# Kernel optimization log

Hardware: AMD Instinct MI355X
Metric: run time of the kernel (lower is better)

The kernel has to match this reference:

```python
import jax, jax.numpy as jnp
import numpy as np

EMBED = 1024
HEADS = 16
HEAD_DIM = EMBED // HEADS
HIDDEN = 4 * EMBED
EPS = 1e-6


def setup_inputs() -> dict:
    key = jax.random.key(0)
    ks = jax.random.split(key, 8)
    s = 0.02
    return {
        "x": jax.random.normal(ks[0], (2, 2048, EMBED), dtype=jnp.float32),
        "ln1_w": jnp.ones((EMBED,), jnp.float32),
        "ln1_b": jnp.zeros((EMBED,), jnp.float32),
        "qkv_w": jax.random.normal(ks[1], (3 * EMBED, EMBED), jnp.float32) * s,
        "qkv_b": jnp.zeros((3 * EMBED,), jnp.float32),
        "proj_w": jax.random.normal(ks[2], (EMBED, EMBED), jnp.float32) * s,
        "proj_b": jnp.zeros((EMBED,), jnp.float32),
        "ln2_w": jnp.ones((EMBED,), jnp.float32),
        "ln2_b": jnp.zeros((EMBED,), jnp.float32),
        "fc1_w": jax.random.normal(ks[3], (HIDDEN, EMBED), jnp.float32) * s,
        "fc1_b": jnp.zeros((HIDDEN,), jnp.float32),
        "fc2_w": jax.random.normal(ks[4], (EMBED, HIDDEN), jnp.float32) * s,
        "fc2_b": jnp.zeros((EMBED,), jnp.float32),
    }


def _layernorm(x, w, b):
    mu = jnp.mean(x, axis=-1, keepdims=True)
    var = jnp.mean(jnp.square(x - mu), axis=-1, keepdims=True)
    return (x - mu) * jax.lax.rsqrt(var + EPS) * w + b


def _attn(x, qkv_w, qkv_b, proj_w, proj_b):
    B, S, E = x.shape
    qkv = x @ qkv_w.T + qkv_b                      # [B,S,3E]
    qkv = qkv.reshape(B, S, 3, HEADS, HEAD_DIM)
    q, k, v = jnp.moveaxis(qkv, 2, 0)              # each [B,S,H,D]
    q = q.transpose(0, 2, 1, 3)                    # [B,H,S,D]
    k = k.transpose(0, 2, 1, 3)
    v = v.transpose(0, 2, 1, 3)
    scale = HEAD_DIM ** -0.5
    scores = jnp.einsum("bhqd,bhkd->bhqk", q, k) * scale
    mask = jnp.tril(jnp.ones((S, S), dtype=bool))
    scores = jnp.where(mask, scores, -jnp.inf)
    attn = jax.nn.softmax(scores, axis=-1)
    out = jnp.einsum("bhqk,bhkd->bhqd", attn, v)   # [B,H,S,D]
    out = out.transpose(0, 2, 1, 3).reshape(B, S, E)
    return out @ proj_w.T + proj_b


def reference(x, ln1_w, ln1_b, qkv_w, qkv_b, proj_w, proj_b,
              ln2_w, ln2_b, fc1_w, fc1_b, fc2_w, fc2_b):
    x = x + _attn(_layernorm(x, ln1_w, ln1_b), qkv_w, qkv_b, proj_w, proj_b)
    h = _layernorm(x, ln2_w, ln2_b)
    h = jax.nn.gelu(h @ fc1_w.T + fc1_b, approximate=False)
    x = x + (h @ fc2_w.T + fc2_b)
    return x
```

## Files before the change

### kernel.cpp

```cpp
#include <hip/hip_runtime.h>
#include <hip/hip_bf16.h>


#define E_    1024
#define TE_   3072
#define S_    2048
#define B_    2
#define H_    16
#define MROWS 4096

typedef __attribute__((ext_vector_type(8))) short bf16x8;
typedef __attribute__((ext_vector_type(4))) short short4v;
typedef __attribute__((ext_vector_type(4))) float f32x4;

__device__ __forceinline__ short f2bf(float f) {
  union { float f; unsigned u; } v; v.f = f;
  unsigned r = v.u + 0x7fffu + ((v.u >> 16) & 1u);
  return (short)(r >> 16);
}
__device__ __forceinline__ float bf2f(short s) {
  union { unsigned u; float f; } v; v.u = ((unsigned)(unsigned short)s) << 16;
  return v.f;
}
__device__ __forceinline__ void gload_lds16(const void* g, void* l) {
  __builtin_amdgcn_global_load_lds(
      (const __attribute__((address_space(1))) unsigned int*)g,
      (__attribute__((address_space(3))) unsigned int*)l, 16, 0, 0);
}
__device__ __forceinline__ float exp2_fast(float x) {
  float r; asm("v_exp_f32 %0, %1" : "=v"(r) : "v"(x)); return r;
}
__device__ __forceinline__ float gelu_f(float v) {
  return 0.5f * v * (1.0f + erff(v * 0.70710678118654752f));
}

__global__ __launch_bounds__(256) void k_cvt4(const float* __restrict__ i0, short* __restrict__ o0, int n0,
                                              const float* __restrict__ i1, short* __restrict__ o1, int n1,
                                              const float* __restrict__ i2, short* __restrict__ o2, int n2,
                                              const float* __restrict__ i3, short* __restrict__ o3, int n3) {
  const float* in; short* out; int n;
  switch (blockIdx.y) {
    case 0: in = i0; out = o0; n = n0; break;
    case 1: in = i1; out = o1; n = n1; break;
    case 2: in = i2; out = o2; n = n2; break;
    default: in = i3; out = o3; n = n3; break;
  }
  int i = blockIdx.x * 256 + threadIdx.x;
  if (i >= n) return;
  float4 v = ((const float4*)in)[i];
  short4v o = { f2bf(v.x), f2bf(v.y), f2bf(v.z), f2bf(v.w) };
  ((short4v*)out)[i] = o;
}

__global__ __launch_bounds__(256) void k_ln(const float* __restrict__ x,
                                            const float* __restrict__ w,
                                            const float* __restrict__ b,
                                            short* __restrict__ out) {
  int row = blockIdx.x;
  int tid = threadIdx.x;
  float4 v = ((const float4*)(x + (size_t)row * E_))[tid];
  float s  = v.x + v.y + v.z + v.w;
  float s2 = v.x*v.x + v.y*v.y + v.z*v.z + v.w*v.w;
  #pragma unroll
  for (int d = 1; d < 64; d <<= 1) { s += __shfl_xor(s, d); s2 += __shfl_xor(s2, d); }
  __shared__ float rs[4], rq[4];
  int wv = tid >> 6;
  if ((tid & 63) == 0) { rs[wv] = s; rq[wv] = s2; }
  __syncthreads();
  s  = rs[0] + rs[1] + rs[2] + rs[3];
  s2 = rq[0] + rq[1] + rq[2] + rq[3];
  float mu  = s * (1.0f / E_);
  float var = fmaxf(s2 * (1.0f / E_) - mu * mu, 0.0f);
  float inv = rsqrtf(var + 1e-6f);
  float4 wv4 = ((const float4*)w)[tid];
  float4 bv4 = ((const float4*)b)[tid];
  short4v o = { f2bf((v.x - mu) * inv * wv4.x + bv4.x),
                f2bf((v.y - mu) * inv * wv4.y + bv4.y),
                f2bf((v.z - mu) * inv * wv4.z + bv4.z),
                f2bf((v.w - mu) * inv * wv4.w + bv4.w) };
  ((short4v*)(out + (size_t)row * E_))[tid] = o;
}

template <int EPI>
__global__ __launch_bounds__(256) void k_gemm(const short* __restrict__ A,
                                              const short* __restrict__ W,
                                              const float* __restrict__ bias,
                                              const float* __restrict__ res,
                                              void* __restrict__ outv,
                                              int M, int N, int K) {
  __shared__ short As[128 * 32];
  __shared__ short Ws[128 * 32];
  int tid  = threadIdx.x;
  int lane = tid & 63, wave = tid >> 6;
  int wm = wave >> 1, wn = wave & 1;
  int m0 = blockIdx.y * 128, n0 = blockIdx.x * 128;
  int fr = lane & 15, fq = lane >> 4, fk = fq * 8;

  f32x4 acc[4][4];
  #pragma unroll
  for (int i = 0; i < 4; ++i)
    #pragma unroll
    for (int j = 0; j < 4; ++j) acc[i][j] = (f32x4){0.f, 0.f, 0.f, 0.f};

  int sr = tid >> 2;
  int sc = (tid & 3) * 8;
  const short* Arow  = A + (size_t)(m0 + sr) * K + sc;
  const short* Wrow  = W + (size_t)(n0 + sr) * K + sc;
  const short* Arow2 = A + (size_t)(m0 + 64 + sr) * K + sc;
  const short* Wrow2 = W + (size_t)(n0 + 64 + sr) * K + sc;
  short* Asl = As + tid * 8;
  short* Wsl = Ws + tid * 8;

  for (int k0 = 0; k0 < K; k0 += 32) {
    __syncthreads();
    gload_lds16(Arow  + k0, Asl);
    gload_lds16(Wrow  + k0, Wsl);
    gload_lds16(Arow2 + k0, Asl + 2048);
    gload_lds16(Wrow2 + k0, Wsl + 2048);
    __syncthreads();
    bf16x8 af[4], bfr[4];
    #pragma unroll
    for (int i = 0; i < 4; ++i) {
      af[i]  = *(const bf16x8*)(As + (wm * 64 + i * 16 + fr) * 32 + fk);
      bfr[i] = *(const bf16x8*)(Ws + (wn * 64 + i * 16 + fr) * 32 + fk);
    }
    #pragma unroll
    for (int mi = 0; mi < 4; ++mi)
      #pragma unroll
      for (int ni = 0; ni < 4; ++ni)
        acc[mi][ni] = __builtin_amdgcn_mfma_f32_16x16x32_bf16(af[mi], bfr[ni],
                                                              acc[mi][ni], 0, 0, 0);
  }

  #pragma unroll
  for (int mi = 0; mi < 4; ++mi) {
    #pragma unroll
    for (int ni = 0; ni < 4; ++ni) {
      int gm0 = m0 + wm * 64 + mi * 16 + fq * 4;
      int gn  = n0 + wn * 64 + ni * 16 + fr;
      float bv = bias[gn];
      #pragma unroll
      for (int j = 0; j < 4; ++j) {
        size_t idx = (size_t)(gm0 + j) * N + gn;
        float v = acc[mi][ni][j] + bv;
        if (EPI == 0)      ((short*)outv)[idx] = f2bf(v);
        else if (EPI == 1) ((float*)outv)[idx] = v + res[idx];
        else               ((short*)outv)[idx] = f2bf(gelu_f(v));
      }
    }
  }
}

__global__ __launch_bounds__(256) void k_attn(const short* __restrict__ qkv,
                                              short* __restrict__ out) {
  __shared__ short Kt[64 * 64];
  __shared__ short Vt[64 * 64];
  __shared__ short Pl[4][1024];
  int tid  = threadIdx.x;
  int lane = tid & 63, w = tid >> 6;
  int qb   = (int)gridDim.x - 1 - (int)blockIdx.x;
  int q0   = qb * 64;
  int bh   = blockIdx.y;
  int b    = bh >> 4, h = bh & 15;
  int fr   = lane & 15, fq = lane >> 4, fk = fq * 8;
  const float sc = 0.18033688011112042f;

  const short* qp = qkv + (size_t)(b * S_ + q0 + w * 16 + fr) * TE_ + h * 64;
  bf16x8 qa0 = *(const bf16x8*)(qp + fk);
  bf16x8 qa1 = *(const bf16x8*)(qp + 32 + fk);

  float m_r = -__builtin_inff();
  float l_r = 0.f;
  f32x4 o[4];
  #pragma unroll
  for (int c = 0; c < 4; ++c) o[c] = (f32x4){0.f, 0.f, 0.f, 0.f};

  int srow = tid >> 3;
  int schunk = tid & 7;
  short* Pw = &Pl[w][0];

  for (int kv = 0; kv <= q0; kv += 64) {
    __syncthreads();
    #pragma unroll
    for (int r = 0; r < 2; ++r) {
      int row = srow + 32 * r;
      size_t grow = (size_t)(b * S_ + kv + row) * TE_ + h * 64;
      gload_lds16(qkv + grow + E_ + ((schunk ^ (srow & 7)) << 3),
                  Kt + r * 2048 + tid * 8);
      bf16x8 vv = *(const bf16x8*)(qkv + grow + 2 * E_ + (schunk << 3));
      int kc = row >> 3, kwi = row & 7;
      #pragma unroll
      for (int j = 0; j < 8; ++j) {
        int d = (schunk << 3) + j;
        int csw = kc ^ (d & 7) ^ ((d >> 3) & 7);
        Vt[d * 64 + csw * 8 + kwi] = vv[j];
      }
    }
    __syncthreads();

    f32x4 s[4];
    #pragma unroll
    for (int g = 0; g < 4; ++g) {
      const short* kb = Kt + ((g << 4) + fr) * 64;
      int sw = fr & 7;
      bf16x8 a0 = *(const bf16x8*)(kb + ((fq ^ sw) << 3));
      bf16x8 a1 = *(const bf16x8*)(kb + (((4 + fq) ^ sw) << 3));
      f32x4 t = (f32x4){0.f, 0.f, 0.f, 0.f};
      t = __builtin_amdgcn_mfma_f32_16x16x32_bf16(a0, qa0, t, 0, 0, 0);
      t = __builtin_amdgcn_mfma_f32_16x16x32_bf16(a1, qa1, t, 0, 0, 0);
      s[g] = t;
    }
    #pragma unroll
    for (int g = 0; g < 4; ++g)
      #pragma unroll
      for (int jj = 0; jj < 4; ++jj) s[g][jj] *= sc;

    if (kv + 64 > q0) {
      int qr = (q0 - kv) + 16 * w + fr;
      #pragma unroll
      for (int g = 0; g < 4; ++g)
        #pragma unroll
        for (int jj = 0; jj < 4; ++jj)
          if (16 * g + 4 * fq + jj > qr) s[g][jj] = -__builtin_inff();
    }

    float mg0 = fmaxf(fmaxf(s[0][0], s[0][1]), fmaxf(s[0][2], s[0][3]));
    float mg1 = fmaxf(fmaxf(s[1][0], s[1][1]), fmaxf(s[1][2], s[1][3]));
    float mg2 = fmaxf(fmaxf(s[2][0], s[2][1]), fmaxf(s[2][2], s[2][3]));
    float mg3 = fmaxf(fmaxf(s[3][0], s[3][1]), fmaxf(s[3][2], s[3][3]));
    float mt = fmaxf(fmaxf(mg0, mg1), fmaxf(mg2, mg3));
    mt = fmaxf(mt, __shfl_xor(mt, 16));
    mt = fmaxf(mt, __shfl_xor(mt, 32));
    float mn = fmaxf(m_r, mt);
    float al = exp2_fast(m_r - mn);
    m_r = mn;
    #pragma unroll
    for (int g = 0; g < 4; ++g)
      #pragma unroll
      for (int jj = 0; jj < 4; ++jj) s[g][jj] = exp2_fast(s[g][jj] - mn);
    f32x4 s4 = s[0] + s[1] + s[2] + s[3];
    float ps = (s4[0] + s4[1]) + (s4[2] + s4[3]);
    ps += __shfl_xor(ps, 16);
    ps += __shfl_xor(ps, 32);
    l_r = l_r * al + ps;

    #pragma unroll
    for (int g = 0; g < 4; ++g) {
      short4v pk = { f2bf(s[g][0]), f2bf(s[g][1]), f2bf(s[g][2]), f2bf(s[g][3]) };
      int pc = (2 * g + (fq >> 1)) ^ (fr & 7);
      *(short4v*)(Pw + fr * 64 + pc * 8 + ((fq & 1) << 2)) = pk;
    }

    #pragma unroll
    for (int c = 0; c < 4; ++c)
      #pragma unroll
      for (int jj = 0; jj < 4; ++jj) o[c][jj] *= al;

    bf16x8 pb0 = *(const bf16x8*)(Pw + fr * 64 + ((fq ^ (fr & 7)) << 3));
    bf16x8 pb1 = *(const bf16x8*)(Pw + fr * 64 + (((4 + fq) ^ (fr & 7)) << 3));
    #pragma unroll
    for (int c = 0; c < 4; ++c) {
      int d = 16 * c + fr;
      int sbase = (d & 7) ^ ((d >> 3) & 7);
      const short* vb = Vt + d * 64;
      bf16x8 va0 = *(const bf16x8*)(vb + ((fq ^ sbase) << 3));
      bf16x8 va1 = *(const bf16x8*)(vb + (((4 + fq) ^ sbase) << 3));
      o[c] = __builtin_amdgcn_mfma_f32_16x16x32_bf16(va0, pb0, o[c], 0, 0, 0);
      o[c] = __builtin_amdgcn_mfma_f32_16x16x32_bf16(va1, pb1, o[c], 0, 0, 0);
    }
  }

  float inv_l = 1.0f / l_r;
  #pragma unroll
  for (int c = 0; c < 4; ++c) {
    short4v okk = { f2bf(o[c][0] * inv_l), f2bf(o[c][1] * inv_l),
                    f2bf(o[c][2] * inv_l), f2bf(o[c][3] * inv_l) };
    int pc = (2 * c + (fq >> 1)) ^ (fr & 7);
    *(short4v*)(Pw + fr * 64 + pc * 8 + ((fq & 1) << 2)) = okk;
  }
  int ql = lane >> 2, dc = lane & 3;
  int swz = ql & 7;
  const short* ob = Pw + ql * 64;
  bf16x8 r0 = *(const bf16x8*)(ob + (((2 * dc) ^ swz) << 3));
  bf16x8 r1 = *(const bf16x8*)(ob + (((2 * dc + 1) ^ swz) << 3));
  short* op = out + (size_t)(b * S_ + q0 + 16 * w + ql) * E_ + h * 64 + dc * 16;
  *(bf16x8*)op = r0;
  *(bf16x8*)(op + 8) = r1;
}

extern "C" void kernel_launch(void* const* d_in, const int* in_sizes, int n_in,
                              void* d_out, int out_size, void* d_ws, size_t ws_size,
                              hipStream_t stream) {
  const float* x      = (const float*)d_in[0];
  const float* ln1_w  = (const float*)d_in[1];
  const float* ln1_b  = (const float*)d_in[2];
  const float* qkv_w  = (const float*)d_in[3];
  const float* qkv_b  = (const float*)d_in[4];
  const float* proj_w = (const float*)d_in[5];
  const float* proj_b = (const float*)d_in[6];
  const float* ln2_w  = (const float*)d_in[7];
  const float* ln2_b  = (const float*)d_in[8];
  const float* fc1_w  = (const float*)d_in[9];
  const float* fc1_b  = (const float*)d_in[10];
  const float* fc2_w  = (const float*)d_in[11];
  const float* fc2_b  = (const float*)d_in[12];
  float* out = (float*)d_out;

  char* ws = (char*)d_ws;
  short* xn1    = (short*)(ws + 0);
  short* qkvb   = (short*)(ws + (8u  << 20));
  short* gelu_o = (short*)(ws + 0);
  short* attn_o = (short*)(ws + (32u << 20));
  short* h_ln2  = (short*)(ws + (32u << 20));
  float* x_res  = (float*)(ws + (40u << 20));
  short* w_qkv  = (short*)(ws + (56u << 20));
  short* w_proj = (short*)(ws + (62u << 20));
  short* w_fc1  = (short*)(ws + (64u << 20));
  short* w_fc2  = (short*)(ws + (72u << 20));

  k_cvt4<<<dim3(4096, 4), 256, 0, stream>>>(qkv_w, w_qkv, 786432,
                                            proj_w, w_proj, 262144,
                                            fc1_w, w_fc1, 1048576,
                                            fc2_w, w_fc2, 1048576);

  k_ln<<<MROWS, 256, 0, stream>>>(x, ln1_w, ln1_b, xn1);
  k_gemm<0><<<dim3(24, 32), 256, 0, stream>>>(xn1, w_qkv, qkv_b, nullptr, qkvb,
                                              MROWS, TE_, E_);
  k_attn<<<dim3(S_ / 64, B_ * H_), 256, 0, stream>>>(qkvb, attn_o);
  k_gemm<1><<<dim3(8, 32), 256, 0, stream>>>(attn_o, w_proj, proj_b, x, x_res,
                                             MROWS, E_, E_);
  k_ln<<<MROWS, 256, 0, stream>>>(x_res, ln2_w, ln2_b, h_ln2);
  k_gemm<2><<<dim3(32, 32), 256, 0, stream>>>(h_ln2, w_fc1, fc1_b, nullptr, gelu_o,
                                              MROWS, 4096, E_);
  k_gemm<1><<<dim3(8, 32), 256, 0, stream>>>(gelu_o, w_fc2, fc2_b, x_res, out,
                                             MROWS, E_, 4096);
}
```

Baseline: 444.1 us.

## Double-buffer GEMM shared-memory tiles to overlap global loads with MFMA

The GEMM main loop now uses two LDS buffers for A and W tiles. It issues the direct global-to-LDS loads for the next K-slice before computing on the current one, so each iteration needs one barrier instead of two. Launch bounds also request three blocks per SM. The cost is twice the LDS per block and possible register pressure from the occupancy hint. There is also a race risk: async LDS loads may need an explicit wait before the barrier.

```diff
diff --git a/kernel.cpp b/kernel.cpp
--- a/kernel.cpp
+++ b/kernel.cpp
@@ -82,14 +82,14 @@
 }
 
 template <int EPI>
-__global__ __launch_bounds__(256) void k_gemm(const short* __restrict__ A,
-                                              const short* __restrict__ W,
-                                              const float* __restrict__ bias,
-                                              const float* __restrict__ res,
-                                              void* __restrict__ outv,
-                                              int M, int N, int K) {
-  __shared__ short As[128 * 32];
-  __shared__ short Ws[128 * 32];
+__global__ __launch_bounds__(256, 3) void k_gemm(const short* __restrict__ A,
+                                                 const short* __restrict__ W,
+                                                 const float* __restrict__ bias,
+                                                 const float* __restrict__ res,
+                                                 void* __restrict__ outv,
+                                                 int M, int N, int K) {
+  __shared__ short As[2][128 * 32];
+  __shared__ short Ws[2][128 * 32];
   int tid  = threadIdx.x;
   int lane = tid & 63, wave = tid >> 6;
   int wm = wave >> 1, wn = wave & 1;
@@ -108,29 +108,45 @@
   const short* Wrow  = W + (size_t)(n0 + sr) * K + sc;
   const short* Arow2 = A + (size_t)(m0 + 64 + sr) * K + sc;
   const short* Wrow2 = W + (size_t)(n0 + 64 + sr) * K + sc;
-  short* Asl = As + tid * 8;
-  short* Wsl = Ws + tid * 8;
-
-  for (int k0 = 0; k0 < K; k0 += 32) {
+
+#define STAGE_(buf, k0)                                   \
+  do {                                                    \
+    gload_lds16(Arow  + (k0), &As[buf][tid * 8]);         \
+    gload_lds16(Arow2 + (k0), &As[buf][2048 + tid * 8]);  \
+    gload_lds16(Wrow  + (k0), &Ws[buf][tid * 8]);         \
+    gload_lds16(Wrow2 + (k0), &Ws[buf][2048 + tid * 8]);  \
+  } while (0)
+
+#define COMPUTE_(buf)                                                         \
+  do {                                                                        \
+    bf16x8 af[4], bfr[4];                                                     \
+    _Pragma("unroll")                                                         \
+    for (int i = 0; i < 4; ++i) {                                             \
+      af[i]  = *(const bf16x8*)(&As[buf][(wm * 64 + i * 16 + fr) * 32 + fk]); \
+      bfr[i] = *(const bf16x8*)(&Ws[buf][(wn * 64 + i * 16 + fr) * 32 + fk]); \
+    }                                                                         \
+    _Pragma("unroll")                                                         \
+    for (int mi = 0; mi < 4; ++mi)                                            \
+      _Pragma("unroll")                                                       \
+      for (int ni = 0; ni < 4; ++ni)                                          \
+        acc[mi][ni] = __builtin_amdgcn_mfma_f32_16x16x32_bf16(                \
+            af[mi], bfr[ni], acc[mi][ni], 0, 0, 0);                           \
+  } while (0)
+
+  int nt = K >> 5;
+  STAGE_(0, 0);
+  __syncthreads();
+  int cur = 0;
+  for (int t = 0; t < nt - 1; ++t) {
+    STAGE_(cur ^ 1, (t + 1) * 32);
+    COMPUTE_(cur);
     __syncthreads();
-    gload_lds16(Arow  + k0, Asl);
-    gload_lds16(Wrow  + k0, Wsl);
-    gload_lds16(Arow2 + k0, Asl + 2048);
-    gload_lds16(Wrow2 + k0, Wsl + 2048);
-    __syncthreads();
-    bf16x8 af[4], bfr[4];
-    #pragma unroll
-    for (int i = 0; i < 4; ++i) {
-      af[i]  = *(const bf16x8*)(As + (wm * 64 + i * 16 + fr) * 32 + fk);
-      bfr[i] = *(const bf16x8*)(Ws + (wn * 64 + i * 16 + fr) * 32 + fk);
-    }
-    #pragma unroll
-    for (int mi = 0; mi < 4; ++mi)
-      #pragma unroll
-      for (int ni = 0; ni < 4; ++ni)
-        acc[mi][ni] = __builtin_amdgcn_mfma_f32_16x16x32_bf16(af[mi], bfr[ni],
-                                                              acc[mi][ni], 0, 0, 0);
-  }
+    cur ^= 1;
+  }
+  COMPUTE_(cur);
+
+#undef STAGE_
+#undef COMPUTE_
 
   #pragma unroll
   for (int mi = 0; mi < 4; ++mi) {
```

New measurement: 413.9 us. 6.8% less time.
